# Optimization experiments

Hardware: AMD Instinct MI355X
Metric: run time of the kernel (lower is better)

## Reference

```python
import jax, jax.numpy as jnp
import numpy as np

N = 50000      # nodes
E = 800000     # edges
P = 200000     # link pairs
D_IN = 128     # input_dim
F_NUM = 128    # filter_num
OUT = 2        # out_dim
K = 10         # APPNP propagation steps
ALPHA = 0.1    # teleport prob


def setup_inputs() -> dict:
    key = jax.random.key(0)
    ks = jax.random.split(key, 9)
    x = jax.random.normal(ks[0], (N, D_IN), dtype=jnp.float32)
    edge_index = jax.random.randint(ks[1], (2, E), 0, N)
    index = jax.random.randint(ks[2], (P, 2), 0, N)
    s1 = 1.0 / np.sqrt(D_IN)
    s2 = 1.0 / np.sqrt(F_NUM)
    s3 = 1.0 / np.sqrt(2 * F_NUM)
    W1 = jax.random.uniform(ks[3], (F_NUM, D_IN), minval=-s1, maxval=s1)
    b1 = jax.random.uniform(ks[4], (F_NUM,), minval=-s1, maxval=s1)
    W2 = jax.random.uniform(ks[5], (F_NUM, F_NUM), minval=-s2, maxval=s2)
    b2 = jax.random.uniform(ks[6], (F_NUM,), minval=-s2, maxval=s2)
    W3 = jax.random.uniform(ks[7], (OUT, 2 * F_NUM), minval=-s3, maxval=s3)
    b3 = jax.random.uniform(ks[8], (OUT,), minval=-s3, maxval=s3)
    return {"x": x, "edge_index": edge_index, "index": index,
            "W1": W1, "b1": b1, "W2": W2, "b2": b2, "W3": W3, "b3": b3}


def _gcn_norm(edge_index, num_nodes):
    # PyG gcn_norm: add self-loops, sym norm D^{-1/2} (A+I) D^{-1/2}
    src, dst = edge_index[0], edge_index[1]
    loop = jnp.arange(num_nodes, dtype=src.dtype)
    src = jnp.concatenate([src, loop])
    dst = jnp.concatenate([dst, loop])
    deg = jax.ops.segment_sum(jnp.ones_like(src, dtype=jnp.float32), dst,
                              num_segments=num_nodes)
    dinv = jnp.where(deg > 0, jax.lax.rsqrt(deg), 0.0)
    norm = dinv[src] * dinv[dst]  # [E+N]
    return src, dst, norm


def _appnp(x, src, dst, norm, num_nodes):
    # h_{k+1} = (1-alpha) * A_hat h_k + alpha * x0
    def step(h, _):
        agg = jax.ops.segment_sum(norm[:, None] * h[src], dst,
                                  num_segments=num_nodes)
        return (1.0 - ALPHA) * agg + ALPHA * x, None
    h, _ = jax.lax.scan(step, x, None, length=K)
    return h


def reference(x, edge_index, index, W1, b1, W2, b2, W3, b3):
    num_nodes = x.shape[0]
    src, dst, norm = _gcn_norm(edge_index, num_nodes)
    h = x @ W1.T + b1                      # [N, F]
    h = jax.nn.relu(_appnp(h, src, dst, norm, num_nodes))
    h = h @ W2.T + b2                      # [N, F]
    h = jax.nn.relu(_appnp(h, src, dst, norm, num_nodes))
    feat = jnp.concatenate([h[index[:, 0]], h[index[:, 1]]], axis=-1)  # [P, 2F]
    out = feat @ W3.T + b3                 # [P, OUT]
    return jax.nn.log_softmax(out, axis=1)
```

## Files before the change

### kernel.cpp

```cpp
#include <hip/hip_runtime.h>
#include <math.h>

#define NN 50000
#define NE 800000
#define NP 200000
#define NF 128
#define NEDGE_TOT (NE + NN)
#define NBLK 196
#define NBK 64
#define DPB 782
#define BKCAP 16384
#define EPB 2048

typedef __attribute__((ext_vector_type(8))) short short8;
typedef __attribute__((ext_vector_type(4))) float float4v;

__device__ __forceinline__ float bf_lo(unsigned u) { return __uint_as_float(u << 16); }
__device__ __forceinline__ float bf_hi(unsigned u) { return __uint_as_float(u & 0xffff0000u); }
__device__ __forceinline__ unsigned short f2bf(float f) {
    unsigned u = __float_as_uint(f);
    return (unsigned short)((u + 0x7fffu + ((u >> 16) & 1u)) >> 16);
}
__device__ __forceinline__ unsigned pack2bf(float a, float b) {
    return (unsigned)f2bf(a) | ((unsigned)f2bf(b) << 16);
}

__global__ __launch_bounds__(256) void init_cnt_k(int* __restrict__ cnt) {
    int i = blockIdx.x * 256 + threadIdx.x;
    if (i < NN) cnt[i] = 1;
}

__global__ __launch_bounds__(256) void count_k(const int* __restrict__ ei,
                                               int* __restrict__ cnt) {
    int e = blockIdx.x * 256 + threadIdx.x;
    if (e < NE) atomicAdd(&cnt[ei[NE + e]], 1);
}

__global__ __launch_bounds__(256) void scan_reduce_k(const int* __restrict__ cnt,
                                                     int* __restrict__ bsum,
                                                     float* __restrict__ dinv) {
    __shared__ int s[256];
    int t = threadIdx.x;
    int idx = blockIdx.x * 256 + t;
    int v = (idx < NN) ? cnt[idx] : 0;
    if (idx < NN) dinv[idx] = rsqrtf((float)v);
    s[t] = v;
    __syncthreads();
    for (int off = 128; off > 0; off >>= 1) {
        if (t < off) s[t] += s[t + off];
        __syncthreads();
    }
    if (t == 0) bsum[blockIdx.x] = s[0];
}

__global__ __launch_bounds__(256) void scan_bsums_k(const int* __restrict__ bsum,
                                                    int* __restrict__ boff) {
    __shared__ int s[256];
    int t = threadIdx.x;
    int v = (t < NBLK) ? bsum[t] : 0;
    s[t] = v;
    __syncthreads();
    for (int off = 1; off < 256; off <<= 1) {
        int add = (t >= off) ? s[t - off] : 0;
        __syncthreads();
        s[t] += add;
        __syncthreads();
    }
    if (t < NBLK) boff[t] = s[t] - v;
}

__global__ __launch_bounds__(256) void scan_down_k(const int* __restrict__ cnt,
                                                   const int* __restrict__ boff,
                                                   int* __restrict__ row_ptr) {
    __shared__ int s[256];
    int t = threadIdx.x;
    int idx = blockIdx.x * 256 + t;
    int v = (idx < NN) ? cnt[idx] : 0;
    s[t] = v;
    __syncthreads();
    for (int off = 1; off < 256; off <<= 1) {
        int add = (t >= off) ? s[t - off] : 0;
        __syncthreads();
        s[t] += add;
        __syncthreads();
    }
    int excl = s[t] - v + boff[blockIdx.x];
    if (idx < NN) {
        row_ptr[idx] = excl;
        if (idx == NN - 1) row_ptr[NN] = excl + v;
    }
}

__global__ __launch_bounds__(256) void bin_k(const int* __restrict__ ei,
                                             int* __restrict__ gtail,
                                             int2* __restrict__ gbk) {
    __shared__ int cntA[NBK], baseA[NBK], gposA[NBK];
    __shared__ int2 stage[EPB];
    int tid = threadIdx.x;
    int ebase = blockIdx.x * EPB;
    int sv[8], dv[8], lp8[8], bk8[8];
    bool val[8];
    if (tid < NBK) cntA[tid] = 0;
    __syncthreads();
#pragma unroll
    for (int k = 0; k < 8; ++k) {
        int e = ebase + k * 256 + tid;
        val[k] = (e < NEDGE_TOT);
        if (val[k]) {
            int s, d;
            if (e < NE) { s = ei[e]; d = ei[NE + e]; }
            else        { s = d = e - NE; }
            sv[k] = s; dv[k] = d;
            bk8[k] = d / DPB;
            lp8[k] = atomicAdd(&cntA[bk8[k]], 1);
        }
    }
    __syncthreads();
    if (tid == 0) {
        int run = 0;
        for (int b = 0; b < NBK; ++b) { baseA[b] = run; run += cntA[b]; }
    }
    __syncthreads();
    if (tid < NBK && cntA[tid] > 0)
        gposA[tid] = atomicAdd(&gtail[tid], cntA[tid]);
    __syncthreads();
#pragma unroll
    for (int k = 0; k < 8; ++k)
        if (val[k]) {
            int2 r; r.x = sv[k]; r.y = dv[k];
            stage[baseA[bk8[k]] + lp8[k]] = r;
        }
    __syncthreads();
    int total = baseA[NBK - 1] + cntA[NBK - 1];
    for (int i = tid; i < total; i += 256) {
        int2 r = stage[i];
        int b = r.y / DPB;
        gbk[(size_t)b * BKCAP + gposA[b] + (i - baseA[b])] = r;
    }
}

__global__ __launch_bounds__(256) void build_k(const int* __restrict__ row_ptr,
                                               const int* __restrict__ gtail,
                                               const int2* __restrict__ gbk,
                                               int* __restrict__ cols) {
    __shared__ int wcur[DPB];
    int tid = threadIdx.x;
    int b = blockIdx.x;
    int d0 = b * DPB;
    for (int i = tid; i < DPB; i += 256) {
        int d = d0 + i;
        wcur[i] = (d < NN) ? row_ptr[d] : 0;
    }
    __syncthreads();
    int nb = gtail[b];
    const int2* src = gbk + (size_t)b * BKCAP;
    for (int t = tid; t < nb; t += 256) {
        int2 r = src[t];
        int pos = atomicAdd(&wcur[r.y - d0], 1);
        cols[pos] = r.x;
    }
}

__global__ __launch_bounds__(256) void zero_k(unsigned short* Ys1, unsigned short* Ys2,
                                              unsigned short* HA, unsigned short* HB,
                                              int* gtail) {
    int t = threadIdx.x;
    unsigned short* bufs[4] = {Ys1, Ys2, HA, HB};
    unsigned short* b = bufs[t >> 6];
    ((unsigned*)(b + (size_t)NN * NF))[t & 63] = 0u;
    if (t < NBK) gtail[t] = 0;
}

__global__ __launch_bounds__(256) void cast_w_k(const float* __restrict__ W,
                                                unsigned short* __restrict__ Wb) {
    int t = blockIdx.x * 256 + threadIdx.x;
    if (t >= 128 * 128 / 8) return;
    int i = t * 8;
    float4 f0 = *(const float4*)(W + i);
    float4 f1 = *(const float4*)(W + i + 4);
    uint4 q;
    q.x = pack2bf(f0.x, f0.y);
    q.y = pack2bf(f0.z, f0.w);
    q.z = pack2bf(f1.x, f1.y);
    q.w = pack2bf(f1.z, f1.w);
    *(uint4*)(Wb + i) = q;
}

#define GPAD 136
template <bool F32IN>
__global__ __launch_bounds__(256) void gemm_mfma_k(const void* __restrict__ Xv,
                                                   const unsigned short* __restrict__ Wb,
                                                   const float* __restrict__ bias,
                                                   const float* __restrict__ dinv,
                                                   unsigned short* __restrict__ Yu,
                                                   unsigned short* __restrict__ Ys,
                                                   int nrows) {
    __shared__ unsigned short sm[4 * 16 * GPAD];
    int wave = threadIdx.x >> 6, lane = threadIdx.x & 63;
    int rbase = blockIdx.x * 64 + wave * 16;
    if (rbase >= nrows) return;
    int quad = lane >> 4, mn = lane & 15;
    float4v acc[8];
#pragma unroll
    for (int ft = 0; ft < 8; ++ft) acc[ft] = (float4v){0.f, 0.f, 0.f, 0.f};
#pragma unroll
    for (int kb = 0; kb < 128; kb += 32) {
        short8 a;
        if (F32IN) {
            const float* X = (const float*)Xv;
            float4 f0 = *(const float4*)(X + (size_t)(rbase + mn) * NF + kb + quad * 8);
            float4 f1 = *(const float4*)(X + (size_t)(rbase + mn) * NF + kb + quad * 8 + 4);
            a[0] = (short)f2bf(f0.x); a[1] = (short)f2bf(f0.y);
            a[2] = (short)f2bf(f0.z); a[3] = (short)f2bf(f0.w);
            a[4] = (short)f2bf(f1.x); a[5] = (short)f2bf(f1.y);
            a[6] = (short)f2bf(f1.z); a[7] = (short)f2bf(f1.w);
        } else {
            const unsigned short* X = (const unsigned short*)Xv;
            a = *(const short8*)(X + (size_t)(rbase + mn) * NF + kb + quad * 8);
        }
#pragma unroll
        for (int ft = 0; ft < 8; ++ft) {
            short8 b = *(const short8*)(Wb + (size_t)(ft * 16 + mn) * NF + kb + quad * 8);
            acc[ft] = __builtin_amdgcn_mfma_f32_16x16x32_bf16(a, b, acc[ft], 0, 0, 0);
        }
    }
    unsigned short* smw = sm + wave * 16 * GPAD;
#pragma unroll
    for (int ft = 0; ft < 8; ++ft) {
        float bv = bias[ft * 16 + mn];
#pragma unroll
        for (int r = 0; r < 4; ++r)
            smw[(quad * 4 + r) * GPAD + ft * 16 + mn] = f2bf(acc[ft][r] + bv);
    }
    __syncthreads();
#pragma unroll
    for (int t = 0; t < 4; ++t) {
        int rl = t * 4 + quad;
        int row = rbase + rl;
        uint4 q = *(const uint4*)(smw + rl * GPAD + mn * 8);
        *(uint4*)(Yu + (size_t)row * NF + mn * 8) = q;
        float g = dinv[row];
        uint4 qs;
        qs.x = pack2bf(g * bf_lo(q.x), g * bf_hi(q.x));
        qs.y = pack2bf(g * bf_lo(q.y), g * bf_hi(q.y));
        qs.z = pack2bf(g * bf_lo(q.z), g * bf_hi(q.z));
        qs.w = pack2bf(g * bf_lo(q.w), g * bf_hi(q.w));
        *(uint4*)(Ys + (size_t)row * NF + mn * 8) = qs;
    }
}

__global__ __launch_bounds__(256) void appnp_s_k(const unsigned short* __restrict__ hs,
                                                 const unsigned short* __restrict__ x0,
                                                 const float* __restrict__ dinv,
                                                 unsigned short* __restrict__ out,
                                                 const int* __restrict__ row_ptr,
                                                 const int* __restrict__ cols,
                                                 int mode,
                                                 const float* __restrict__ W3,
                                                 float4* __restrict__ puv) {
    int wid = (blockIdx.x * 256 + threadIdx.x) >> 6;
    int lane = threadIdx.x & 63;
    if (wid >= NN) return;
    int half = lane >> 5, li = lane & 31;
    int beg = row_ptr[wid], end = row_ptr[wid + 1];
    float a0 = 0.f, a1 = 0.f, a2 = 0.f, a3 = 0.f;
    for (int e = beg; e < end; e += 64) {
        int m = end - e;
        if (m > 64) m = 64;
        int c = (lane < m) ? cols[e + lane] : NN;
        for (int j = 0; j < m; j += 8) {
#pragma unroll
            for (int p = 0; p < 4; ++p) {
                int cj = __shfl(c, j + 2 * p + half, 64);
                uint2 q = *((const uint2*)(hs + (size_t)cj * NF) + li);
                a0 += bf_lo(q.x);
                a1 += bf_hi(q.x);
                a2 += bf_lo(q.y);
                a3 += bf_hi(q.y);
            }
        }
    }
    a0 += __shfl_xor(a0, 32, 64);
    a1 += __shfl_xor(a1, 32, 64);
    a2 += __shfl_xor(a2, 32, 64);
    a3 += __shfl_xor(a3, 32, 64);
    if (half == 0) {
        float g = dinv[wid];
        float s9 = 0.9f * g;
        uint2 xq = *((const uint2*)(x0 + (size_t)wid * NF) + li);
        float h0 = s9 * a0 + 0.1f * bf_lo(xq.x);
        float h1 = s9 * a1 + 0.1f * bf_hi(xq.x);
        float h2 = s9 * a2 + 0.1f * bf_lo(xq.y);
        float h3 = s9 * a3 + 0.1f * bf_hi(xq.y);
        if (mode == 0) {
            uint2 oq;
            oq.x = pack2bf(g * h0, g * h1);
            oq.y = pack2bf(g * h2, g * h3);
            *((uint2*)(out + (size_t)wid * NF) + li) = oq;
        } else {
            h0 = fmaxf(h0, 0.f); h1 = fmaxf(h1, 0.f);
            h2 = fmaxf(h2, 0.f); h3 = fmaxf(h3, 0.f);
            if (mode == 1) {
                uint2 oq;
                oq.x = pack2bf(h0, h1);
                oq.y = pack2bf(h2, h3);
                *((uint2*)(out + (size_t)wid * NF) + li) = oq;
            } else {
                int fb = li * 4;
                float4 wu0 = *(const float4*)(W3 + fb);
                float4 wv0 = *(const float4*)(W3 + 128 + fb);
                float4 wu1 = *(const float4*)(W3 + 256 + fb);
                float4 wv1 = *(const float4*)(W3 + 384 + fb);
                float du0 = h0 * wu0.x + h1 * wu0.y + h2 * wu0.z + h3 * wu0.w;
                float du1 = h0 * wu1.x + h1 * wu1.y + h2 * wu1.z + h3 * wu1.w;
                float dv0 = h0 * wv0.x + h1 * wv0.y + h2 * wv0.z + h3 * wv0.w;
                float dv1 = h0 * wv1.x + h1 * wv1.y + h2 * wv1.z + h3 * wv1.w;
#pragma unroll
                for (int off = 1; off < 32; off <<= 1) {
                    du0 += __shfl_xor(du0, off, 64);
                    du1 += __shfl_xor(du1, off, 64);
                    dv0 += __shfl_xor(dv0, off, 64);
                    dv1 += __shfl_xor(dv1, off, 64);
                }
                if (li == 0) puv[wid] = make_float4(du0, du1, dv0, dv1);
            }
        }
    }
}

__global__ __launch_bounds__(256) void pair2_k(const float4* __restrict__ puv,
                                               const int2* __restrict__ index,
                                               const float* __restrict__ b3,
                                               float* __restrict__ outp) {
    int p = blockIdx.x * 256 + threadIdx.x;
    if (p >= NP) return;
    int2 uv = index[p];
    float4 a = puv[uv.x];
    float4 b = puv[uv.y];
    float s0 = a.x + b.z + b3[0];
    float s1 = a.y + b.w + b3[1];
    float m = fmaxf(s0, s1);
    float lse = m + logf(expf(s0 - m) + expf(s1 - m));
    *(float2*)(outp + (size_t)p * 2) = make_float2(s0 - lse, s1 - lse);
}

extern "C" void kernel_launch(void* const* d_in, const int* in_sizes, int n_in,
                              void* d_out, int out_size, void* d_ws, size_t ws_size,
                              hipStream_t stream) {
    const float* x  = (const float*)d_in[0];
    const int* ei   = (const int*)d_in[1];
    const int* idx  = (const int*)d_in[2];
    const float* W1 = (const float*)d_in[3];
    const float* b1 = (const float*)d_in[4];
    const float* W2 = (const float*)d_in[5];
    const float* b2 = (const float*)d_in[6];
    const float* W3 = (const float*)d_in[7];
    const float* b3 = (const float*)d_in[8];
    float* out = (float*)d_out;

    char* ws = (char*)d_ws;
    size_t off = 0;
    auto alloc = [&](size_t bytes) -> void* {
        void* p = ws + off;
        off = (off + bytes + 255) & ~(size_t)255;
        return p;
    };
    const size_t HROWS = (size_t)(NN + 1) * NF;
    int*   cnt     = (int*)  alloc(NN * sizeof(int));
    float* dinv    = (float*)alloc(NN * sizeof(float));
    int*   row_ptr = (int*)  alloc((NN + 1) * sizeof(int));
    int*   bsum    = (int*)  alloc(NBLK * sizeof(int));
    int*   boff    = (int*)  alloc(NBLK * sizeof(int));
    int*   gtail   = (int*)  alloc(NBK * sizeof(int));
    int2*  gbk     = (int2*) alloc((size_t)NBK * BKCAP * sizeof(int2));
    int*   cols    = (int*)  alloc((size_t)NEDGE_TOT * sizeof(int));
    float4* puv    = (float4*)alloc((size_t)NN * sizeof(float4));
    unsigned short* Wb1 = (unsigned short*)alloc(128 * 128 * 2);
    unsigned short* Wb2 = (unsigned short*)alloc(128 * 128 * 2);
    unsigned short* Yu1 = (unsigned short*)alloc(HROWS * 2);
    unsigned short* Ys1 = (unsigned short*)alloc(HROWS * 2);
    unsigned short* Yu2 = (unsigned short*)alloc(HROWS * 2);
    unsigned short* Ys2 = (unsigned short*)alloc(HROWS * 2);
    unsigned short* HA  = (unsigned short*)alloc(HROWS * 2);
    unsigned short* HB  = (unsigned short*)alloc(HROWS * 2);
    unsigned short* Hrelu = (unsigned short*)alloc((size_t)NN * NF * 2);

    const int gN    = (NN + 255) / 256;
    const int gE    = (NE + 255) / 256;
    const int gBin  = (NEDGE_TOT + EPB - 1) / EPB;
    const int gGemm = (NN + 63) / 64;
    const int gStep = (NN * 64 + 255) / 256;
    const int gPair = (NP + 255) / 256;

    cast_w_k<<<8, 256, 0, stream>>>(W1, Wb1);
    cast_w_k<<<8, 256, 0, stream>>>(W2, Wb2);
    zero_k<<<1, 256, 0, stream>>>(Ys1, Ys2, HA, HB, gtail);
    init_cnt_k<<<gN, 256, 0, stream>>>(cnt);
    count_k<<<gE, 256, 0, stream>>>(ei, cnt);
    scan_reduce_k<<<NBLK, 256, 0, stream>>>(cnt, bsum, dinv);
    scan_bsums_k<<<1, 256, 0, stream>>>(bsum, boff);
    scan_down_k<<<NBLK, 256, 0, stream>>>(cnt, boff, row_ptr);
    bin_k<<<gBin, 256, 0, stream>>>(ei, gtail, gbk);
    build_k<<<NBK, 256, 0, stream>>>(row_ptr, gtail, gbk, cols);

    gemm_mfma_k<true><<<gGemm, 256, 0, stream>>>(x, Wb1, b1, dinv, Yu1, Ys1, NN);
    {
        const unsigned short* cur = Ys1;
        for (int k = 0; k < 10; ++k) {
            unsigned short* dst = (k == 9) ? Hrelu : ((k & 1) ? HB : HA);
            appnp_s_k<<<gStep, 256, 0, stream>>>(cur, Yu1, dinv, dst, row_ptr,
                                                 cols, (k == 9) ? 1 : 0, W3, puv);
            cur = dst;
        }
    }
    gemm_mfma_k<false><<<gGemm, 256, 0, stream>>>(Hrelu, Wb2, b2, dinv, Yu2, Ys2, NN);
    {
        const unsigned short* cur = Ys2;
        for (int k = 0; k < 10; ++k) {
            unsigned short* dst = (k & 1) ? HB : HA;
            appnp_s_k<<<gStep, 256, 0, stream>>>(cur, Yu2, dinv, dst, row_ptr,
                                                 cols, (k == 9) ? 2 : 0, W3, puv);
            cur = dst;
        }
    }
    pair2_k<<<gPair, 256, 0, stream>>>(puv, (const int2*)idx, b3, out);
}
```

Baseline: 832.3 us.

## Quantize propagated APPNP features to int8 with per-node scales

Stores the dinv-prescaled intermediate features used in APPNP propagation as int8 with a per-row float scale instead of bf16. A separate quantize kernel runs after each GEMM, and each propagation step requantizes its output. Gather lanes are regrouped so 16 lanes cover a 128-byte row, with four neighbours per wave pass. This halves the bytes gathered per edge in the bandwidth-bound sparse aggregation, at the cost of int8 precision loss that compounds over 20 steps, extra dequant and scale arithmetic, and one extra kernel per layer.

```diff
diff --git a/kernel.cpp b/kernel.cpp
--- a/kernel.cpp
+++ b/kernel.cpp
@@ -23,6 +23,9 @@
 }
 __device__ __forceinline__ unsigned pack2bf(float a, float b) {
     return (unsigned)f2bf(a) | ((unsigned)f2bf(b) << 16);
+}
+__device__ __forceinline__ float i8f(unsigned v, int sh) {
+    return (float)(signed char)(v >> sh);
 }
 
 __global__ __launch_bounds__(256) void init_cnt_k(int* __restrict__ cnt) {
@@ -161,14 +164,18 @@
     }
 }
 
-__global__ __launch_bounds__(256) void zero_k(unsigned short* Ys1, unsigned short* Ys2,
-                                              unsigned short* HA, unsigned short* HB,
+__global__ __launch_bounds__(256) void zero_k(unsigned char* QA, unsigned char* QB,
+                                              unsigned char* QC,
+                                              float* sA, float* sB, float* sC,
                                               int* gtail) {
     int t = threadIdx.x;
-    unsigned short* bufs[4] = {Ys1, Ys2, HA, HB};
-    unsigned short* b = bufs[t >> 6];
-    ((unsigned*)(b + (size_t)NN * NF))[t & 63] = 0u;
-    if (t < NBK) gtail[t] = 0;
+    unsigned char* bufs[3] = {QA, QB, QC};
+    if (t < 96)
+        ((unsigned*)(bufs[t >> 5] + (size_t)NN * NF))[t & 31] = 0u;
+    if (t == 96) sA[NN] = 0.f;
+    if (t == 97) sB[NN] = 0.f;
+    if (t == 98) sC[NN] = 0.f;
+    if (t >= 128 && t < 128 + NBK) gtail[t - 128] = 0;
 }
 
 __global__ __launch_bounds__(256) void cast_w_k(const float* __restrict__ W,
@@ -191,9 +198,7 @@
 __global__ __launch_bounds__(256) void gemm_mfma_k(const void* __restrict__ Xv,
                                                    const unsigned short* __restrict__ Wb,
                                                    const float* __restrict__ bias,
-                                                   const float* __restrict__ dinv,
                                                    unsigned short* __restrict__ Yu,
-                                                   unsigned short* __restrict__ Ys,
                                                    int nrows) {
     __shared__ unsigned short sm[4 * 16 * GPAD];
     int wave = threadIdx.x >> 6, lane = threadIdx.x & 63;
@@ -236,23 +241,51 @@
 #pragma unroll
     for (int t = 0; t < 4; ++t) {
         int rl = t * 4 + quad;
-        int row = rbase + rl;
         uint4 q = *(const uint4*)(smw + rl * GPAD + mn * 8);
-        *(uint4*)(Yu + (size_t)row * NF + mn * 8) = q;
-        float g = dinv[row];
-        uint4 qs;
-        qs.x = pack2bf(g * bf_lo(q.x), g * bf_hi(q.x));
-        qs.y = pack2bf(g * bf_lo(q.y), g * bf_hi(q.y));
-        qs.z = pack2bf(g * bf_lo(q.z), g * bf_hi(q.z));
-        qs.w = pack2bf(g * bf_lo(q.w), g * bf_hi(q.w));
-        *(uint4*)(Ys + (size_t)row * NF + mn * 8) = qs;
-    }
-}
-
-__global__ __launch_bounds__(256) void appnp_s_k(const unsigned short* __restrict__ hs,
+        *(uint4*)(Yu + (size_t)(rbase + rl) * NF + mn * 8) = q;
+    }
+}
+
+__global__ __launch_bounds__(256) void quant_k(const unsigned short* __restrict__ Yu,
+                                               const float* __restrict__ dinv,
+                                               unsigned char* __restrict__ Q,
+                                               float* __restrict__ scl) {
+    int node = (blockIdx.x * 256 + threadIdx.x) >> 4;
+    int li = threadIdx.x & 15;
+    if (node >= NN) return;
+    float g = dinv[node];
+    uint4 xq = *((const uint4*)(Yu + (size_t)node * NF) + li);
+    float h0 = g * bf_lo(xq.x), h1 = g * bf_hi(xq.x);
+    float h2 = g * bf_lo(xq.y), h3 = g * bf_hi(xq.y);
+    float h4 = g * bf_lo(xq.z), h5 = g * bf_hi(xq.z);
+    float h6 = g * bf_lo(xq.w), h7 = g * bf_hi(xq.w);
+    float mx = fmaxf(fmaxf(fmaxf(fabsf(h0), fabsf(h1)), fmaxf(fabsf(h2), fabsf(h3))),
+                     fmaxf(fmaxf(fabsf(h4), fabsf(h5)), fmaxf(fabsf(h6), fabsf(h7))));
+#pragma unroll
+    for (int off = 1; off < 16; off <<= 1)
+        mx = fmaxf(mx, __shfl_xor(mx, off, 64));
+    float smax = fmaxf(mx, 1e-20f);
+    float inv = 127.0f / smax;
+    uint2 q;
+    q.x = ((unsigned)((int)rintf(h0 * inv)) & 255u)
+        | ((unsigned)((int)rintf(h1 * inv)) & 255u) << 8
+        | ((unsigned)((int)rintf(h2 * inv)) & 255u) << 16
+        | ((unsigned)((int)rintf(h3 * inv)) & 255u) << 24;
+    q.y = ((unsigned)((int)rintf(h4 * inv)) & 255u)
+        | ((unsigned)((int)rintf(h5 * inv)) & 255u) << 8
+        | ((unsigned)((int)rintf(h6 * inv)) & 255u) << 16
+        | ((unsigned)((int)rintf(h7 * inv)) & 255u) << 24;
+    *((uint2*)(Q + (size_t)node * NF) + li) = q;
+    if (li == 0) scl[node] = smax * (1.0f / 127.0f);
+}
+
+__global__ __launch_bounds__(256) void appnp_q_k(const unsigned char* __restrict__ Q,
+                                                 const float* __restrict__ scl,
                                                  const unsigned short* __restrict__ x0,
                                                  const float* __restrict__ dinv,
-                                                 unsigned short* __restrict__ out,
+                                                 unsigned char* __restrict__ oQ,
+                                                 float* __restrict__ oscl,
+                                                 unsigned short* __restrict__ outbf,
                                                  const int* __restrict__ row_ptr,
                                                  const int* __restrict__ cols,
                                                  int mode,
@@ -261,69 +294,114 @@
     int wid = (blockIdx.x * 256 + threadIdx.x) >> 6;
     int lane = threadIdx.x & 63;
     if (wid >= NN) return;
-    int half = lane >> 5, li = lane & 31;
+    int g4 = lane >> 4, li = lane & 15;
     int beg = row_ptr[wid], end = row_ptr[wid + 1];
     float a0 = 0.f, a1 = 0.f, a2 = 0.f, a3 = 0.f;
+    float a4 = 0.f, a5 = 0.f, a6 = 0.f, a7 = 0.f;
     for (int e = beg; e < end; e += 64) {
         int m = end - e;
         if (m > 64) m = 64;
         int c = (lane < m) ? cols[e + lane] : NN;
+        float sv = scl[c];
         for (int j = 0; j < m; j += 8) {
-#pragma unroll
-            for (int p = 0; p < 4; ++p) {
-                int cj = __shfl(c, j + 2 * p + half, 64);
-                uint2 q = *((const uint2*)(hs + (size_t)cj * NF) + li);
-                a0 += bf_lo(q.x);
-                a1 += bf_hi(q.x);
-                a2 += bf_lo(q.y);
-                a3 += bf_hi(q.y);
+            int cj0 = __shfl(c, j + g4, 64);
+            float sj0 = __shfl(sv, j + g4, 64);
+            int cj1 = __shfl(c, j + 4 + g4, 64);
+            float sj1 = __shfl(sv, j + 4 + g4, 64);
+            uint2 q0 = *((const uint2*)(Q + (size_t)cj0 * NF) + li);
+            uint2 q1 = *((const uint2*)(Q + (size_t)cj1 * NF) + li);
+            a0 += sj0 * i8f(q0.x, 0);  a1 += sj0 * i8f(q0.x, 8);
+            a2 += sj0 * i8f(q0.x, 16); a3 += sj0 * i8f(q0.x, 24);
+            a4 += sj0 * i8f(q0.y, 0);  a5 += sj0 * i8f(q0.y, 8);
+            a6 += sj0 * i8f(q0.y, 16); a7 += sj0 * i8f(q0.y, 24);
+            a0 += sj1 * i8f(q1.x, 0);  a1 += sj1 * i8f(q1.x, 8);
+            a2 += sj1 * i8f(q1.x, 16); a3 += sj1 * i8f(q1.x, 24);
+            a4 += sj1 * i8f(q1.y, 0);  a5 += sj1 * i8f(q1.y, 8);
+            a6 += sj1 * i8f(q1.y, 16); a7 += sj1 * i8f(q1.y, 24);
+        }
+    }
+#pragma unroll
+    for (int off = 16; off < 64; off <<= 1) {
+        a0 += __shfl_xor(a0, off, 64);
+        a1 += __shfl_xor(a1, off, 64);
+        a2 += __shfl_xor(a2, off, 64);
+        a3 += __shfl_xor(a3, off, 64);
+        a4 += __shfl_xor(a4, off, 64);
+        a5 += __shfl_xor(a5, off, 64);
+        a6 += __shfl_xor(a6, off, 64);
+        a7 += __shfl_xor(a7, off, 64);
+    }
+    if (g4 != 0) return;
+    float g = dinv[wid];
+    float s9 = 0.9f * g;
+    uint4 xq = *((const uint4*)(x0 + (size_t)wid * NF) + li);
+    float h0 = s9 * a0 + 0.1f * bf_lo(xq.x);
+    float h1 = s9 * a1 + 0.1f * bf_hi(xq.x);
+    float h2 = s9 * a2 + 0.1f * bf_lo(xq.y);
+    float h3 = s9 * a3 + 0.1f * bf_hi(xq.y);
+    float h4 = s9 * a4 + 0.1f * bf_lo(xq.z);
+    float h5 = s9 * a5 + 0.1f * bf_hi(xq.z);
+    float h6 = s9 * a6 + 0.1f * bf_lo(xq.w);
+    float h7 = s9 * a7 + 0.1f * bf_hi(xq.w);
+    if (mode == 0) {
+        h0 *= g; h1 *= g; h2 *= g; h3 *= g;
+        h4 *= g; h5 *= g; h6 *= g; h7 *= g;
+        float mx = fmaxf(fmaxf(fmaxf(fabsf(h0), fabsf(h1)), fmaxf(fabsf(h2), fabsf(h3))),
+                         fmaxf(fmaxf(fabsf(h4), fabsf(h5)), fmaxf(fabsf(h6), fabsf(h7))));
+#pragma unroll
+        for (int off = 1; off < 16; off <<= 1)
+            mx = fmaxf(mx, __shfl_xor(mx, off, 64));
+        float smax = fmaxf(mx, 1e-20f);
+        float inv = 127.0f / smax;
+        uint2 q;
+        q.x = ((unsigned)((int)rintf(h0 * inv)) & 255u)
+            | ((unsigned)((int)rintf(h1 * inv)) & 255u) << 8
+            | ((unsigned)((int)rintf(h2 * inv)) & 255u) << 16
+            | ((unsigned)((int)rintf(h3 * inv)) & 255u) << 24;
+        q.y = ((unsigned)((int)rintf(h4 * inv)) & 255u)
+            | ((unsigned)((int)rintf(h5 * inv)) & 255u) << 8
+            | ((unsigned)((int)rintf(h6 * inv)) & 255u) << 16
+            | ((unsigned)((int)rintf(h7 * inv)) & 255u) << 24;
+        *((uint2*)(oQ + (size_t)wid * NF) + li) = q;
+        if (li == 0) oscl[wid] = smax * (1.0f / 127.0f);
+    } else {
+        h0 = fmaxf(h0, 0.f); h1 = fmaxf(h1, 0.f);
+        h2 = fmaxf(h2, 0.f); h3 = fmaxf(h3, 0.f);
+        h4 = fmaxf(h4, 0.f); h5 = fmaxf(h5, 0.f);
+        h6 = fmaxf(h6, 0.f); h7 = fmaxf(h7, 0.f);
+        if (mode == 1) {
+            uint4 oq;
+            oq.x = pack2bf(h0, h1);
+            oq.y = pack2bf(h2, h3);
+            oq.z = pack2bf(h4, h5);
+            oq.w = pack2bf(h6, h7);
+            *((uint4*)(outbf + (size_t)wid * NF) + li) = oq;
+        } else {
+            int fb = li * 8;
+            float4 wu0a = *(const float4*)(W3 + fb);
+            float4 wu0b = *(const float4*)(W3 + fb + 4);
+            float4 wv0a = *(const float4*)(W3 + 128 + fb);
+            float4 wv0b = *(const float4*)(W3 + 128 + fb + 4);
+            float4 wu1a = *(const float4*)(W3 + 256 + fb);
+            float4 wu1b = *(const float4*)(W3 + 256 + fb + 4);
+            float4 wv1a = *(const float4*)(W3 + 384 + fb);
+            float4 wv1b = *(const float4*)(W3 + 384 + fb + 4);
+            float du0 = h0 * wu0a.x + h1 * wu0a.y + h2 * wu0a.z + h3 * wu0a.w
+                      + h4 * wu0b.x + h5 * wu0b.y + h6 * wu0b.z + h7 * wu0b.w;
+            float du1 = h0 * wu1a.x + h1 * wu1a.y + h2 * wu1a.z + h3 * wu1a.w
+                      + h4 * wu1b.x + h5 * wu1b.y + h6 * wu1b.z + h7 * wu1b.w;
+            float dv0 = h0 * wv0a.x + h1 * wv0a.y + h2 * wv0a.z + h3 * wv0a.w
+                      + h4 * wv0b.x + h5 * wv0b.y + h6 * wv0b.z + h7 * wv0b.w;
+            float dv1 = h0 * wv1a.x + h1 * wv1a.y + h2 * wv1a.z + h3 * wv1a.w
+                      + h4 * wv1b.x + h5 * wv1b.y + h6 * wv1b.z + h7 * wv1b.w;
+#pragma unroll
+            for (int off = 1; off < 16; off <<= 1) {
+                du0 += __shfl_xor(du0, off, 64);
+                du1 += __shfl_xor(du1, off, 64);
+                dv0 += __shfl_xor(dv0, off, 64);
+                dv1 += __shfl_xor(dv1, off, 64);
             }
-        }
-    }
-    a0 += __shfl_xor(a0, 32, 64);
-    a1 += __shfl_xor(a1, 32, 64);
-    a2 += __shfl_xor(a2, 32, 64);
-    a3 += __shfl_xor(a3, 32, 64);
-    if (half == 0) {
-        float g = dinv[wid];
-        float s9 = 0.9f * g;
-        uint2 xq = *((const uint2*)(x0 + (size_t)wid * NF) + li);
-        float h0 = s9 * a0 + 0.1f * bf_lo(xq.x);
-        float h1 = s9 * a1 + 0.1f * bf_hi(xq.x);
-        float h2 = s9 * a2 + 0.1f * bf_lo(xq.y);
-        float h3 = s9 * a3 + 0.1f * bf_hi(xq.y);
-        if (mode == 0) {
-            uint2 oq;
-            oq.x = pack2bf(g * h0, g * h1);
-            oq.y = pack2bf(g * h2, g * h3);
-            *((uint2*)(out + (size_t)wid * NF) + li) = oq;
-        } else {
-            h0 = fmaxf(h0, 0.f); h1 = fmaxf(h1, 0.f);
-            h2 = fmaxf(h2, 0.f); h3 = fmaxf(h3, 0.f);
-            if (mode == 1) {
-                uint2 oq;
-                oq.x = pack2bf(h0, h1);
-                oq.y = pack2bf(h2, h3);
-                *((uint2*)(out + (size_t)wid * NF) + li) = oq;
-            } else {
-                int fb = li * 4;
-                float4 wu0 = *(const float4*)(W3 + fb);
-                float4 wv0 = *(const float4*)(W3 + 128 + fb);
-                float4 wu1 = *(const float4*)(W3 + 256 + fb);
-                float4 wv1 = *(const float4*)(W3 + 384 + fb);
-                float du0 = h0 * wu0.x + h1 * wu0.y + h2 * wu0.z + h3 * wu0.w;
-                float du1 = h0 * wu1.x + h1 * wu1.y + h2 * wu1.z + h3 * wu1.w;
-                float dv0 = h0 * wv0.x + h1 * wv0.y + h2 * wv0.z + h3 * wv0.w;
-                float dv1 = h0 * wv1.x + h1 * wv1.y + h2 * wv1.z + h3 * wv1.w;
-#pragma unroll
-                for (int off = 1; off < 32; off <<= 1) {
-                    du0 += __shfl_xor(du0, off, 64);
-                    du1 += __shfl_xor(du1, off, 64);
-                    dv0 += __shfl_xor(dv0, off, 64);
-                    dv1 += __shfl_xor(dv1, off, 64);
-                }
-                if (li == 0) puv[wid] = make_float4(du0, du1, dv0, dv1);
-            }
+            if (li == 0) puv[wid] = make_float4(du0, du1, dv0, dv1);
         }
     }
 }
@@ -365,7 +443,7 @@
         off = (off + bytes + 255) & ~(size_t)255;
         return p;
     };
-    const size_t HROWS = (size_t)(NN + 1) * NF;
+    const size_t QROWS = (size_t)(NN + 1) * NF;
     int*   cnt     = (int*)  alloc(NN * sizeof(int));
     float* dinv    = (float*)alloc(NN * sizeof(float));
     int*   row_ptr = (int*)  alloc((NN + 1) * sizeof(int));
@@ -377,24 +455,27 @@
     float4* puv    = (float4*)alloc((size_t)NN * sizeof(float4));
     unsigned short* Wb1 = (unsigned short*)alloc(128 * 128 * 2);
     unsigned short* Wb2 = (unsigned short*)alloc(128 * 128 * 2);
-    unsigned short* Yu1 = (unsigned short*)alloc(HROWS * 2);
-    unsigned short* Ys1 = (unsigned short*)alloc(HROWS * 2);
-    unsigned short* Yu2 = (unsigned short*)alloc(HROWS * 2);
-    unsigned short* Ys2 = (unsigned short*)alloc(HROWS * 2);
-    unsigned short* HA  = (unsigned short*)alloc(HROWS * 2);
-    unsigned short* HB  = (unsigned short*)alloc(HROWS * 2);
+    unsigned short* Yu1 = (unsigned short*)alloc((size_t)NN * NF * 2);
+    unsigned short* Yu2 = (unsigned short*)alloc((size_t)NN * NF * 2);
     unsigned short* Hrelu = (unsigned short*)alloc((size_t)NN * NF * 2);
+    unsigned char* QA = (unsigned char*)alloc(QROWS);
+    unsigned char* QB = (unsigned char*)alloc(QROWS);
+    unsigned char* QC = (unsigned char*)alloc(QROWS);
+    float* sA = (float*)alloc((NN + 1) * sizeof(float));
+    float* sB = (float*)alloc((NN + 1) * sizeof(float));
+    float* sC = (float*)alloc((NN + 1) * sizeof(float));
 
     const int gN    = (NN + 255) / 256;
     const int gE    = (NE + 255) / 256;
     const int gBin  = (NEDGE_TOT + EPB - 1) / EPB;
     const int gGemm = (NN + 63) / 64;
+    const int gQnt  = (NN * 16 + 255) / 256;
     const int gStep = (NN * 64 + 255) / 256;
     const int gPair = (NP + 255) / 256;
 
     cast_w_k<<<8, 256, 0, stream>>>(W1, Wb1);
     cast_w_k<<<8, 256, 0, stream>>>(W2, Wb2);
-    zero_k<<<1, 256, 0, stream>>>(Ys1, Ys2, HA, HB, gtail);
+    zero_k<<<1, 256, 0, stream>>>(QA, QB, QC, sA, sB, sC, gtail);
     init_cnt_k<<<gN, 256, 0, stream>>>(cnt);
     count_k<<<gE, 256, 0, stream>>>(ei, cnt);
     scan_reduce_k<<<NBLK, 256, 0, stream>>>(cnt, bsum, dinv);
@@ -403,24 +484,31 @@
     bin_k<<<gBin, 256, 0, stream>>>(ei, gtail, gbk);
     build_k<<<NBK, 256, 0, stream>>>(row_ptr, gtail, gbk, cols);
 
-    gemm_mfma_k<true><<<gGemm, 256, 0, stream>>>(x, Wb1, b1, dinv, Yu1, Ys1, NN);
+    unsigned char* Qs[3] = {QA, QB, QC};
+    float* ss[3] = {sA, sB, sC};
+
+    gemm_mfma_k<true><<<gGemm, 256, 0, stream>>>(x, Wb1, b1, Yu1, NN);
+    quant_k<<<gQnt, 256, 0, stream>>>(Yu1, dinv, QA, sA);
     {
-        const unsigned short* cur = Ys1;
+        int cur = 0;
         for (int k = 0; k < 10; ++k) {
-            unsigned short* dst = (k == 9) ? Hrelu : ((k & 1) ? HB : HA);
-            appnp_s_k<<<gStep, 256, 0, stream>>>(cur, Yu1, dinv, dst, row_ptr,
-                                                 cols, (k == 9) ? 1 : 0, W3, puv);
-            cur = dst;
-        }
-    }
-    gemm_mfma_k<false><<<gGemm, 256, 0, stream>>>(Hrelu, Wb2, b2, dinv, Yu2, Ys2, NN);
+            int nxt = (k & 1) ? 2 : 1;
+            appnp_q_k<<<gStep, 256, 0, stream>>>(
+                Qs[cur], ss[cur], Yu1, dinv, Qs[nxt], ss[nxt], Hrelu,
+                row_ptr, cols, (k == 9) ? 1 : 0, W3, puv);
+            cur = nxt;
+        }
+    }
+    gemm_mfma_k<false><<<gGemm, 256, 0, stream>>>(Hrelu, Wb2, b2, Yu2, NN);
+    quant_k<<<gQnt, 256, 0, stream>>>(Yu2, dinv, QA, sA);
     {
-        const unsigned short* cur = Ys2;
+        int cur = 0;
         for (int k = 0; k < 10; ++k) {
-            unsigned short* dst = (k & 1) ? HB : HA;
-            appnp_s_k<<<gStep, 256, 0, stream>>>(cur, Yu2, dinv, dst, row_ptr,
-                                                 cols, (k == 9) ? 2 : 0, W3, puv);
-            cur = dst;
+            int nxt = (k & 1) ? 2 : 1;
+            appnp_q_k<<<gStep, 256, 0, stream>>>(
+                Qs[cur], ss[cur], Yu2, dinv, Qs[nxt], ss[nxt], Hrelu,
+                row_ptr, cols, (k == 9) ? 2 : 0, W3, puv);
+            cur = nxt;
         }
     }
     pair2_k<<<gPair, 256, 0, stream>>>(puv, (const int2*)idx, b3, out);
```

After: 833.8 us. About the same (+0.2%).
